# Performance work log

Hardware: AMD Instinct MI355X
Metric: run time of the kernel (lower is better)

The kernel has to match this reference:

```python
import jax, jax.numpy as jnp
import numpy as np

B, T, D, H, K = 2, 2048, 1024, 16, 4
DH = D // H  # 64 head dim
EPS_L2 = 1e-6
EPS_RMS = 1e-6


def setup_inputs() -> dict:
    key = jax.random.key(0)
    ks = jax.random.split(key, 10)
    s = 0.02
    return {
        'x': jax.random.normal(ks[0], (B, T, D), jnp.float32),
        'Wq': jax.random.normal(ks[1], (D, D), jnp.float32) * s,
        'Wk': jax.random.normal(ks[2], (D, D), jnp.float32) * s,
        'Wv': jax.random.normal(ks[3], (D, D), jnp.float32) * s,
        'Wb': jax.random.normal(ks[4], (D, H), jnp.float32) * s,
        'conv_q': jax.random.normal(ks[5], (D, K), jnp.float32) * 0.5,
        'conv_k': jax.random.normal(ks[6], (D, K), jnp.float32) * 0.5,
        'conv_v': jax.random.normal(ks[7], (D, K), jnp.float32) * 0.5,
        'rms_g': jnp.ones((DH,), jnp.float32),
        'Wo': jax.random.normal(ks[8], (D, D), jnp.float32) * s,
    }


def _silu(u):
    return u * jax.nn.sigmoid(u)


def _short_conv(x, w):
    # causal depthwise conv1d, x: [B,T,C], w: [C,K]; y[t] = sum_i w[:,i]*x[t-(K-1)+i]
    k = w.shape[1]
    xp = jnp.pad(x, ((0, 0), (k - 1, 0), (0, 0)))
    y = xp[:, 0:T, :] * w[:, 0]
    for i in range(1, k):
        y = y + xp[:, i:i + T, :] * w[:, i]
    return y


def _l2norm(u):
    return u * jax.lax.rsqrt(jnp.sum(u * u, axis=-1, keepdims=True) + EPS_L2)


def reference(x, Wq, Wk, Wv, Wb, conv_q, conv_k, conv_v, rms_g, Wo):
    # projections + causal short conv (silu fused, as in fla ShortConvolution)
    q = _silu(_short_conv(x @ Wq, conv_q)).reshape(B, T, H, DH)
    k = _silu(_short_conv(x @ Wk, conv_k)).reshape(B, T, H, DH)
    v = _silu(_short_conv(x @ Wv, conv_v)).reshape(B, T, H, DH)
    q = _l2norm(q)
    k = _l2norm(k)
    beta = jax.nn.sigmoid(x @ Wb)  # [B,T,H]

    # time-major for scan
    qs = q.transpose(1, 0, 2, 3)  # [T,B,H,DH]
    ks_ = k.transpose(1, 0, 2, 3)
    vs = v.transpose(1, 0, 2, 3)
    bs = beta.transpose(1, 0, 2)  # [T,B,H]

    def step(S, inp):
        # S: [B,H,dk,dv]; delta rule: S <- S + beta * k (v - k^T S)^T
        q_t, k_t, v_t, b_t = inp
        kS = jnp.einsum('bhk,bhkv->bhv', k_t, S)
        S = S + jnp.einsum('bhk,bhv->bhkv', k_t, b_t[..., None] * (v_t - kS))
        o_t = jnp.einsum('bhk,bhkv->bhv', q_t, S)
        return S, o_t

    S0 = jnp.zeros((B, H, DH, DH), x.dtype)
    _, o = jax.lax.scan(step, S0, (qs, ks_, vs, bs))  # o: [T,B,H,DH]
    o = o.transpose(1, 0, 2, 3)  # [B,T,H,DH]

    # per-head RMSNorm then output projection
    o = o * jax.lax.rsqrt(jnp.mean(o * o, axis=-1, keepdims=True) + EPS_RMS) * rms_g
    return o.reshape(B, T, D) @ Wo
```

## Files before the change

### kernel.cpp

```cpp
#include <hip/hip_runtime.h>
#include <hip/hip_bf16.h>
#include <math.h>

#define B_ 2
#define T_ 2048
#define D_ 1024
#define H_ 16
#define DH_ 64
#define M_ (B_*T_)
#define NC_ 32
#define CS_ 64
#define NCH_ (B_*H_*NC_)
#define QKVN_ 3072

typedef __attribute__((ext_vector_type(4))) float floatx4;
typedef __attribute__((ext_vector_type(8))) short short8;

__device__ __forceinline__ ushort f2bf(float f) {
  union { float f; unsigned u; } c; c.f = f;
  unsigned r = (c.u + 0x7FFFu + ((c.u >> 16) & 1u)) >> 16;
  return (ushort)r;
}
__device__ __forceinline__ float siluf(float u) {
  return u / (1.f + __expf(-u));
}
__device__ __forceinline__ float f4get(const float4& v, int j) {
  return j == 0 ? v.x : j == 1 ? v.y : j == 2 ? v.z : v.w;
}
__device__ __forceinline__ float rdlane(float v, int l) {
  return __int_as_float(__builtin_amdgcn_readlane(__float_as_int(v), l));
}
__device__ __forceinline__ int ksw(int r, int c) { return ((c ^ (r >> 4)) << 2); }

__global__ void cast_kernel(const float* __restrict__ in, ushort* __restrict__ out, int n4) {
  int i = blockIdx.x * blockDim.x + threadIdx.x;
  if (i >= n4) return;
  float4 v = ((const float4*)in)[i];
  ushort4 o;
  o.x = f2bf(v.x); o.y = f2bf(v.y); o.z = f2bf(v.z); o.w = f2bf(v.w);
  ((ushort4*)out)[i] = o;
}

__global__ void transpose_cast_kernel(const float* __restrict__ W, ushort* __restrict__ Wt,
                                      int K, int N) {
  __shared__ float tile[32][33];
  int tx = threadIdx.x, ty = threadIdx.y;
  int n0 = blockIdx.x * 32, k0 = blockIdx.y * 32;
  #pragma unroll
  for (int i = 0; i < 32; i += 8)
    tile[ty + i][tx] = W[(size_t)(k0 + ty + i) * N + n0 + tx];
  __syncthreads();
  #pragma unroll
  for (int i = 0; i < 32; i += 8)
    Wt[(size_t)(n0 + ty + i) * K + k0 + tx] = f2bf(tile[tx][ty + i]);
}

__global__ void transpose_wb_kernel(const float* __restrict__ Wb, float* __restrict__ WbT) {
  int bk = blockIdx.x;
  int tid = threadIdx.x;
  int kl = tid >> 4, h = tid & 15;
  int k = bk * 16 + kl;
  WbT[(size_t)h * D_ + k] = Wb[(size_t)k * H_ + h];
}

__global__ __launch_bounds__(256) void gemm128_kernel(
    const ushort* __restrict__ A, const ushort* __restrict__ Bt,
    float* __restrict__ C, int M, int N, int K) {
  __shared__ ushort lA[128 * 32];
  __shared__ ushort lB[128 * 32];
  int tid = threadIdx.x;
  int wave = tid >> 6, lane = tid & 63;
  int wm = wave >> 1, wn = wave & 1;
  int m16 = lane & 15, q4 = lane >> 4;
  int bm = blockIdx.x, bn = blockIdx.y;
  floatx4 acc[4][4] = {};
  int srow = tid >> 2;
  int sk8 = tid & 3;
  const ushort* Ag = A + (size_t)(bm * 128 + srow) * K + sk8 * 8;
  const ushort* Bg = Bt + (size_t)(bn * 128 + srow) * K + sk8 * 8;
  ushort* lAp = lA + tid * 8;
  ushort* lBp = lB + tid * 8;
  for (int k0 = 0; k0 < K; k0 += 32) {
    __builtin_amdgcn_global_load_lds(
        (const __attribute__((address_space(1))) void*)(Ag + k0),
        (__attribute__((address_space(3))) void*)lAp, 16, 0, 0);
    __builtin_amdgcn_global_load_lds(
        (const __attribute__((address_space(1))) void*)(Ag + (size_t)64 * K + k0),
        (__attribute__((address_space(3))) void*)(lAp + 2048), 16, 0, 0);
    __builtin_amdgcn_global_load_lds(
        (const __attribute__((address_space(1))) void*)(Bg + k0),
        (__attribute__((address_space(3))) void*)lBp, 16, 0, 0);
    __builtin_amdgcn_global_load_lds(
        (const __attribute__((address_space(1))) void*)(Bg + (size_t)64 * K + k0),
        (__attribute__((address_space(3))) void*)(lBp + 2048), 16, 0, 0);
    __syncthreads();
    short8 af[4], bf[4];
    #pragma unroll
    for (int i = 0; i < 4; i++) {
      af[i] = *(short8*)&lA[(wm * 64 + i * 16 + m16) * 32 + q4 * 8];
      bf[i] = *(short8*)&lB[(wn * 64 + i * 16 + m16) * 32 + q4 * 8];
    }
    #pragma unroll
    for (int mi = 0; mi < 4; mi++)
      #pragma unroll
      for (int nj = 0; nj < 4; nj++)
        acc[mi][nj] = __builtin_amdgcn_mfma_f32_16x16x32_bf16(af[mi], bf[nj], acc[mi][nj], 0, 0, 0);
    __syncthreads();
  }
  float* Cb = C + (size_t)(bm * 128) * N + bn * 128;
  #pragma unroll
  for (int mi = 0; mi < 4; mi++) {
    #pragma unroll
    for (int nj = 0; nj < 4; nj++) {
      #pragma unroll
      for (int i = 0; i < 4; i++) {
        int row = wm * 64 + mi * 16 + q4 * 4 + i;
        int col = wn * 64 + nj * 16 + m16;
        Cb[(size_t)row * N + col] = acc[mi][nj][i];
      }
    }
  }
}

__global__ __launch_bounds__(256) void beta_kernel(const float* __restrict__ x,
                                                   const float* __restrict__ WbT,
                                                   float* __restrict__ beta) {
  __shared__ __align__(16) float xs[D_];
  int row = blockIdx.x;
  int tid = threadIdx.x;
  ((float4*)xs)[tid] = ((const float4*)(x + (size_t)row * D_))[tid];
  __syncthreads();
  int h = tid >> 4;
  int seg = tid & 15;
  const float4* wrow = (const float4*)(WbT + (size_t)h * D_) + seg * 16;
  const float4* xsrow = (const float4*)xs + seg * 16;
  float s = 0.f;
  #pragma unroll
  for (int j = 0; j < 16; j++) {
    int jj = (j + seg) & 15;
    float4 xv = xsrow[jj];
    float4 wv = wrow[jj];
    s += xv.x * wv.x + xv.y * wv.y + xv.z * wv.z + xv.w * wv.w;
  }
  #pragma unroll
  for (int off = 8; off; off >>= 1) s += __shfl_down(s, off, 16);
  if (seg == 0) beta[(size_t)row * H_ + h] = 1.f / (1.f + __expf(-s));
}

__global__ __launch_bounds__(256) void conv_kernel(
    const float* __restrict__ qkv,
    const float* __restrict__ cq, const float* __restrict__ ck, const float* __restrict__ cv,
    float* __restrict__ qo, float* __restrict__ ko, float* __restrict__ vo) {
  int row = blockIdx.x;
  int t = row & (T_ - 1);
  int tid = threadIdx.x;
  int c0 = tid * 4;
  float4 zf = {0.f, 0.f, 0.f, 0.f};
  float4 xq[4], xk[4], xv[4];
  #pragma unroll
  for (int i = 0; i < 4; i++) {
    int tt = t - 3 + i;
    if (tt >= 0) {
      const float* rp = qkv + (size_t)(row - 3 + i) * QKVN_;
      xq[i] = *(const float4*)(rp + c0);
      xk[i] = *(const float4*)(rp + 1024 + c0);
      xv[i] = *(const float4*)(rp + 2048 + c0);
    } else { xq[i] = zf; xk[i] = zf; xv[i] = zf; }
  }
  float yq[4], yk[4], yv[4];
  float pq = 0.f, pk = 0.f;
  #pragma unroll
  for (int j = 0; j < 4; j++) {
    float4 wq = ((const float4*)cq)[c0 + j];
    float4 wk = ((const float4*)ck)[c0 + j];
    float4 wv = ((const float4*)cv)[c0 + j];
    float sq = 0.f, sk = 0.f, sv = 0.f;
    #pragma unroll
    for (int i = 0; i < 4; i++) {
      sq += f4get(wq, i) * f4get(xq[i], j);
      sk += f4get(wk, i) * f4get(xk[i], j);
      sv += f4get(wv, i) * f4get(xv[i], j);
    }
    yq[j] = siluf(sq); yk[j] = siluf(sk); yv[j] = siluf(sv);
    pq += yq[j] * yq[j]; pk += yk[j] * yk[j];
  }
  #pragma unroll
  for (int off = 1; off < 16; off <<= 1) {
    pq += __shfl_xor(pq, off, 16);
    pk += __shfl_xor(pk, off, 16);
  }
  float rq = rsqrtf(pq + 1e-6f), rk = rsqrtf(pk + 1e-6f);
  float4 oq = {yq[0]*rq, yq[1]*rq, yq[2]*rq, yq[3]*rq};
  float4 okk = {yk[0]*rk, yk[1]*rk, yk[2]*rk, yk[3]*rk};
  float4 ov = {yv[0], yv[1], yv[2], yv[3]};
  *(float4*)(qo + (size_t)row * D_ + c0) = oq;
  *(float4*)(ko + (size_t)row * D_ + c0) = okk;
  *(float4*)(vo + (size_t)row * D_ + c0) = ov;
}

__global__ __launch_bounds__(256) void prep1_kernel(
    const float* __restrict__ kn, const float* __restrict__ vn,
    const float* __restrict__ beta,
    float* __restrict__ Wkbuf, float* __restrict__ U0buf) {
  __shared__ __align__(16) float Ash[64 * 68];
  __shared__ float bsh[64];
  __shared__ __align__(16) float uni[5312];
  float (*Ksh)[68] = (float (*)[68])uni;
  float (*Tsh)[16][20] = (float (*)[16][20])uni;
  float (*Msh)[16][20] = (float (*)[16][20])(uni + 1280);
  float (*Xsh)[132] = (float (*)[132])(uni + 3200);

  int ch = blockIdx.x;
  int b = ch >> 9, h = (ch >> 5) & 15, c = ch & 31;
  int tid = threadIdx.x;
  int t = tid >> 2, seg = tid & 3;
  int wave = tid >> 6, lane = tid & 63;
  int r = lane >> 2, q = lane & 3;
  const float* krow = kn + ((size_t)(b * T_ + c * 64 + t)) * D_ + h * 64;
  #pragma unroll
  for (int g = 0; g < 4; g++)
    *(float4*)&Ksh[t][ksw(t, seg * 4 + g)] = *(const float4*)&krow[seg * 16 + 4 * g];
  if (tid < 64) bsh[tid] = beta[((size_t)(b * T_ + c * 64 + tid)) * H_ + h];
  __syncthreads();
  {
    int s0 = seg * 16;
    float acc[16];
    #pragma unroll
    for (int rr = 0; rr < 16; rr++) acc[rr] = 0.f;
    for (int d4 = 0; d4 < 16; d4++) {
      float4 kt = *(float4*)&Ksh[t][ksw(t, d4)];
      #pragma unroll
      for (int rr = 0; rr < 16; rr++) {
        float4 ks = *(float4*)&Ksh[s0 + rr][((d4 ^ seg) << 2)];
        acc[rr] += kt.x * ks.x + kt.y * ks.y + kt.z * ks.z + kt.w * ks.w;
      }
    }
    float bt = bsh[t];
    #pragma unroll
    for (int g = 0; g < 4; g++) {
      float4 a4;
      a4.x = (t > s0 + 4*g + 0) ? bt * acc[4*g+0] : 0.f;
      a4.y = (t > s0 + 4*g + 1) ? bt * acc[4*g+1] : 0.f;
      a4.z = (t > s0 + 4*g + 2) ? bt * acc[4*g+2] : 0.f;
      a4.w = (t > s0 + 4*g + 3) ? bt * acc[4*g+3] : 0.f;
      *(float4*)&Ash[t * 68 + s0 + 4 * g] = a4;
    }
  }
  float xk[16], xv[16];
  {
    float bt = bsh[t];
    const float* vrow = vn + ((size_t)(b * T_ + c * 64 + t)) * D_ + h * 64;
    #pragma unroll
    for (int g = 0; g < 4; g++) {
      float4 kv = *(float4*)&Ksh[t][ksw(t, seg * 4 + g)];
      float4 vv = *(const float4*)&vrow[seg * 16 + 4 * g];
      xk[4*g+0] = bt * kv.x; xk[4*g+1] = bt * kv.y; xk[4*g+2] = bt * kv.z; xk[4*g+3] = bt * kv.w;
      xv[4*g+0] = bt * vv.x; xv[4*g+1] = bt * vv.y; xv[4*g+2] = bt * vv.z; xv[4*g+3] = bt * vv.w;
    }
  }
  __syncthreads();
  {
    float a[16];
    #pragma unroll
    for (int i = 0; i < 16; i++) a[i] = Ash[(wave * 16 + r) * 68 + wave * 16 + i];
    float4 w4 = {0.f, 0.f, 0.f, 0.f};
    if ((r >> 2) == q) ((float*)&w4)[r & 3] = 1.f;
    #pragma unroll
    for (int i = 0; i < 15; i++) {
      int src = i * 4 + q;
      float4 wi;
      wi.x = __shfl(w4.x, src, 64);
      wi.y = __shfl(w4.y, src, 64);
      wi.z = __shfl(w4.z, src, 64);
      wi.w = __shfl(w4.w, src, 64);
      if (r > i) {
        w4.x -= a[i] * wi.x; w4.y -= a[i] * wi.y;
        w4.z -= a[i] * wi.z; w4.w -= a[i] * wi.w;
      }
    }
    *(float4*)&Tsh[wave][r][q * 4] = w4;
  }
  __syncthreads();
  for (int k = 0; k < wave; k++) {
    float4 m4 = {0.f, 0.f, 0.f, 0.f};
    #pragma unroll
    for (int i = 0; i < 16; i++) {
      float aik = Ash[(wave * 16 + r) * 68 + k * 16 + i];
      float4 tk = *(float4*)&Tsh[k][i][q * 4];
      m4.x += aik * tk.x; m4.y += aik * tk.y;
      m4.z += aik * tk.z; m4.w += aik * tk.w;
    }
    int mi = wave * (wave - 1) / 2 + k;
    *(float4*)&Msh[mi][r][q * 4] = m4;
  }
  float* wkout = &Wkbuf[(size_t)ch * 4096 + t * 64];
  float* u0out = &U0buf[(size_t)ch * 4096 + t * 64];
  for (int k = 0; k < 4; k++) {
    if (wave == k) {
      #pragma unroll
      for (int g = 0; g < 4; g++) {
        float4 k4 = {xk[4*g+0], xk[4*g+1], xk[4*g+2], xk[4*g+3]};
        float4 v4 = {xv[4*g+0], xv[4*g+1], xv[4*g+2], xv[4*g+3]};
        *(float4*)&Xsh[r][seg * 16 + 4 * g] = k4;
        *(float4*)&Xsh[r][64 + seg * 16 + 4 * g] = v4;
      }
    }
    __syncthreads();
    if (wave == k) {
      float nk[16], nv[16];
      #pragma unroll
      for (int i2 = 0; i2 < 16; i2++) { nk[i2] = 0.f; nv[i2] = 0.f; }
      #pragma unroll
      for (int i = 0; i < 16; i++) {
        float tc = Tsh[k][r][i];
        #pragma unroll
        for (int g = 0; g < 4; g++) {
          float4 yk = *(float4*)&Xsh[i][seg * 16 + 4 * g];
          float4 yv = *(float4*)&Xsh[i][64 + seg * 16 + 4 * g];
          nk[4*g+0] += tc * yk.x; nk[4*g+1] += tc * yk.y;
          nk[4*g+2] += tc * yk.z; nk[4*g+3] += tc * yk.w;
          nv[4*g+0] += tc * yv.x; nv[4*g+1] += tc * yv.y;
          nv[4*g+2] += tc * yv.z; nv[4*g+3] += tc * yv.w;
        }
      }
      #pragma unroll
      for (int g = 0; g < 4; g++) {
        float4 k4 = {nk[4*g+0], nk[4*g+1], nk[4*g+2], nk[4*g+3]};
        float4 v4 = {nv[4*g+0], nv[4*g+1], nv[4*g+2], nv[4*g+3]};
        *(float4*)&wkout[seg * 16 + 4 * g] = k4;
        *(float4*)&u0out[seg * 16 + 4 * g] = v4;
      }
    } else if (wave > k) {
      int mi = wave * (wave - 1) / 2 + k;
      #pragma unroll
      for (int i = 0; i < 16; i++) {
        float mc = Msh[mi][r][i];
        #pragma unroll
        for (int g = 0; g < 4; g++) {
          float4 yk = *(float4*)&Xsh[i][seg * 16 + 4 * g];
          float4 yv = *(float4*)&Xsh[i][64 + seg * 16 + 4 * g];
          xk[4*g+0] -= mc * yk.x; xk[4*g+1] -= mc * yk.y;
          xk[4*g+2] -= mc * yk.z; xk[4*g+3] -= mc * yk.w;
          xv[4*g+0] -= mc * yv.x; xv[4*g+1] -= mc * yv.y;
          xv[4*g+2] -= mc * yv.z; xv[4*g+3] -= mc * yv.w;
        }
      }
    }
    __syncthreads();
  }
}

__global__ __launch_bounds__(256) void prep2a_kernel(
    const float* __restrict__ qn, const float* __restrict__ kn,
    float* __restrict__ Lbuf) {
  __shared__ float Qsh[64][68];
  __shared__ float Ksh[64][68];
  int ch = blockIdx.x;
  int b = ch >> 9, h = (ch >> 5) & 15, c = ch & 31;
  int tid = threadIdx.x;
  int t = tid >> 2, seg = tid & 3;
  const float* qrow = qn + ((size_t)(b * T_ + c * 64 + t)) * D_ + h * 64;
  const float* krow = kn + ((size_t)(b * T_ + c * 64 + t)) * D_ + h * 64;
  #pragma unroll
  for (int g = 0; g < 4; g++) {
    *(float4*)&Qsh[t][seg * 16 + 4 * g] = *(const float4*)&qrow[seg * 16 + 4 * g];
    *(float4*)&Ksh[t][ksw(t, seg * 4 + g)] = *(const float4*)&krow[seg * 16 + 4 * g];
  }
  __syncthreads();
  int s0 = seg * 16;
  float acc[16];
  #pragma unroll
  for (int r = 0; r < 16; r++) acc[r] = 0.f;
  for (int d4 = 0; d4 < 16; d4++) {
    float4 qt = *(float4*)&Qsh[t][d4 * 4];
    #pragma unroll
    for (int r = 0; r < 16; r++) {
      float4 ks = *(float4*)&Ksh[s0 + r][((d4 ^ seg) << 2)];
      acc[r] += qt.x * ks.x + qt.y * ks.y + qt.z * ks.z + qt.w * ks.w;
    }
  }
  #pragma unroll
  for (int g = 0; g < 4; g++) {
    float4 ov;
    ov.x = (s0 + 4*g + 0 <= t) ? acc[4*g+0] : 0.f;
    ov.y = (s0 + 4*g + 1 <= t) ? acc[4*g+1] : 0.f;
    ov.z = (s0 + 4*g + 2 <= t) ? acc[4*g+2] : 0.f;
    ov.w = (s0 + 4*g + 3 <= t) ? acc[4*g+3] : 0.f;
    *(float4*)&Lbuf[(size_t)ch * 4096 + t * 64 + s0 + 4 * g] = ov;
  }
}

__global__ __launch_bounds__(256) void prep2b_kernel(
    const float* __restrict__ Lbuf, const float* __restrict__ Wkbuf,
    const float* __restrict__ U0buf, float* qn,
    float* __restrict__ O0buf) {
  __shared__ float Lsh[64][68];
  __shared__ float Wksh[64][68];
  __shared__ float U0sh[64][68];
  int ch = blockIdx.x;
  int b = ch >> 9, h = (ch >> 5) & 15, c = ch & 31;
  int tid = threadIdx.x;
  int t = tid >> 2, seg = tid & 3;
  #pragma unroll
  for (int g = 0; g < 4; g++) {
    int o = t * 64 + seg * 16 + 4 * g;
    *(float4*)&Lsh[t][seg * 16 + 4 * g]  = *(const float4*)&Lbuf[(size_t)ch * 4096 + o];
    *(float4*)&Wksh[t][seg * 16 + 4 * g] = *(const float4*)&Wkbuf[(size_t)ch * 4096 + o];
    *(float4*)&U0sh[t][seg * 16 + 4 * g] = *(const float4*)&U0buf[(size_t)ch * 4096 + o];
  }
  __syncthreads();
  int j0 = seg * 16;
  float o0[16], lw[16];
  #pragma unroll
  for (int r = 0; r < 16; r++) { o0[r] = 0.f; lw[r] = 0.f; }
  for (int s = 0; s <= t; s++) {
    float l = Lsh[t][s];
    #pragma unroll
    for (int g = 0; g < 4; g++) {
      float4 u = *(float4*)&U0sh[s][j0 + 4 * g];
      float4 w = *(float4*)&Wksh[s][j0 + 4 * g];
      o0[4*g+0] += l * u.x; o0[4*g+1] += l * u.y; o0[4*g+2] += l * u.z; o0[4*g+3] += l * u.w;
      lw[4*g+0] += l * w.x; lw[4*g+1] += l * w.y; lw[4*g+2] += l * w.z; lw[4*g+3] += l * w.w;
    }
  }
  float* qrow = qn + ((size_t)(b * T_ + c * 64 + t)) * D_ + h * 64;
  #pragma unroll
  for (int g = 0; g < 4; g++) {
    float4 qv = *(const float4*)&qrow[j0 + 4 * g];
    qv.x -= lw[4*g+0]; qv.y -= lw[4*g+1]; qv.z -= lw[4*g+2]; qv.w -= lw[4*g+3];
    *(float4*)&qrow[j0 + 4 * g] = qv;
    float4 ov = {o0[4*g+0], o0[4*g+1], o0[4*g+2], o0[4*g+3]};
    *(float4*)&O0buf[(size_t)ch * 4096 + t * 64 + j0 + 4 * g] = ov;
  }
}

__global__ __launch_bounds__(256) void prep2c_kernel(
    float* kn, const float* __restrict__ Wkbuf,
    const float* __restrict__ U0buf, float* __restrict__ Pbuf) {
  __shared__ float Ksh[64][68];
  __shared__ float Wksh[64][68];
  __shared__ float U0sh[64][68];
  int ch = blockIdx.x;
  int b = ch >> 9, h = (ch >> 5) & 15, c = ch & 31;
  int tid = threadIdx.x;
  int t = tid >> 2, seg = tid & 3;
  const float* krow = kn + ((size_t)(b * T_ + c * 64 + t)) * D_ + h * 64;
  #pragma unroll
  for (int g = 0; g < 4; g++) {
    int o = t * 64 + seg * 16 + 4 * g;
    *(float4*)&Ksh[t][seg * 16 + 4 * g]  = *(const float4*)&krow[seg * 16 + 4 * g];
    *(float4*)&Wksh[t][seg * 16 + 4 * g] = *(const float4*)&Wkbuf[(size_t)ch * 4096 + o];
    *(float4*)&U0sh[t][seg * 16 + 4 * g] = *(const float4*)&U0buf[(size_t)ch * 4096 + o];
  }
  __syncthreads();
  int d0 = seg * 16;
  float accP[16], accZ[16];
  #pragma unroll
  for (int r = 0; r < 16; r++) { accP[r] = 0.f; accZ[r] = 0.f; }
  for (int s = 0; s < 64; s++) {
    float kt = Ksh[s][t];
    float u  = U0sh[s][t];
    #pragma unroll
    for (int g = 0; g < 4; g++) {
      float4 w4 = *(float4*)&Wksh[s][d0 + 4 * g];
      float4 k4 = *(float4*)&Ksh[s][d0 + 4 * g];
      accP[4*g+0] += kt * w4.x; accP[4*g+1] += kt * w4.y; accP[4*g+2] += kt * w4.z; accP[4*g+3] += kt * w4.w;
      accZ[4*g+0] += u * k4.x;  accZ[4*g+1] += u * k4.y;  accZ[4*g+2] += u * k4.z;  accZ[4*g+3] += u * k4.w;
    }
  }
  float* zrow = kn + ((size_t)(b * T_ + c * 64 + t)) * D_ + h * 64;
  #pragma unroll
  for (int g = 0; g < 4; g++) {
    float4 pv;
    pv.x = ((d0 + 4*g + 0) == t ? 1.f : 0.f) - accP[4*g+0];
    pv.y = ((d0 + 4*g + 1) == t ? 1.f : 0.f) - accP[4*g+1];
    pv.z = ((d0 + 4*g + 2) == t ? 1.f : 0.f) - accP[4*g+2];
    pv.w = ((d0 + 4*g + 3) == t ? 1.f : 0.f) - accP[4*g+3];
    *(float4*)&Pbuf[(size_t)ch * 4096 + (size_t)(seg * 4 + g) * 256 + (size_t)t * 4] = pv;
    float4 zv = {accZ[4*g+0], accZ[4*g+1], accZ[4*g+2], accZ[4*g+3]};
    *(float4*)&zrow[d0 + 4 * g] = zv;
  }
}

__global__ __launch_bounds__(256) void state_kernel(
    const float* __restrict__ kn , const float* __restrict__ Pbuf ,
    float* __restrict__ Sbuf) {
  __shared__ __align__(16) float Pl[2][4096];
  int bid = blockIdx.x;
  int bh = bid & 31, js = bid >> 5;
  int h = bh & 15, b = bh >> 4;
  int tid = threadIdx.x;
  int wv = tid >> 6, lane = tid & 63;
  int j0 = js * 4 + wv;
  float s0 = 0.f;
  const size_t bhNC = (size_t)bh * NC_;
  const float* Pg0 = Pbuf + bhNC * 4096;
  #pragma unroll
  for (int g = 0; g < 4; g++)
    __builtin_amdgcn_global_load_lds(
        (const __attribute__((address_space(1))) void*)(Pg0 + (g * 256 + tid) * 4),
        (__attribute__((address_space(3))) void*)&Pl[0][(g * 256 + tid) * 4], 16, 0, 0);
  float zn = kn[((size_t)(b * T_ + j0)) * D_ + h * 64 + lane];
  int cur = 0;
  #pragma unroll 1
  for (int c = 0; c < NC_; c++) {
    __syncthreads();
    float z = zn;
    size_t ch = bhNC + c;
    if (c + 1 < NC_) {
      const float* Pg = Pbuf + (ch + 1) * 4096;
      #pragma unroll
      for (int g = 0; g < 4; g++)
        __builtin_amdgcn_global_load_lds(
            (const __attribute__((address_space(1))) void*)(Pg + (g * 256 + tid) * 4),
            (__attribute__((address_space(3))) void*)&Pl[cur ^ 1][(g * 256 + tid) * 4], 16, 0, 0);
      zn = kn[((size_t)(b * T_ + (c + 1) * 64 + j0)) * D_ + h * 64 + lane];
    }
    Sbuf[ch * 4096 + (size_t)j0 * 64 + lane] = s0;
    float acc = z;
    #pragma unroll
    for (int f = 0; f < 16; f++) {
      floatx4 pv = *(floatx4*)&Pl[cur][f * 256 + lane * 4];
      acc += pv.x * rdlane(s0, f * 4 + 0);
      acc += pv.y * rdlane(s0, f * 4 + 1);
      acc += pv.z * rdlane(s0, f * 4 + 2);
      acc += pv.w * rdlane(s0, f * 4 + 3);
    }
    s0 = acc;
    cur ^= 1;
  }
}

__global__ __launch_bounds__(256) void ophase_kernel(
    const float* __restrict__ qn , const float* __restrict__ Sbuf,
    const float* __restrict__ O0buf, const float* __restrict__ rms_g,
    ushort* __restrict__ ob) {
  __shared__ float Ssht[64][68];
  __shared__ float QshT[64][65];
  __shared__ float part[64][4];
  int ch = blockIdx.x;
  int b = ch >> 9, h = (ch >> 5) & 15, c = ch & 31;
  int tid = threadIdx.x;
  int t = tid & 63, jg = tid >> 6;
  #pragma unroll
  for (int g = 0; g < 4; g++) {
    int idx = tid + g * 256;
    *(float4*)&Ssht[idx >> 4][(idx & 15) * 4] =
        *(const float4*)&Sbuf[(size_t)ch * 4096 + (size_t)idx * 4];
  }
  #pragma unroll
  for (int g = 0; g < 4; g++) {
    int idx = tid + g * 256;
    int row = idx >> 4, c4 = idx & 15;
    float4 qv = *(const float4*)&qn[((size_t)(b * T_ + c * 64 + row)) * D_ + h * 64 + c4 * 4];
    QshT[c4 * 4 + 0][row] = qv.x;
    QshT[c4 * 4 + 1][row] = qv.y;
    QshT[c4 * 4 + 2][row] = qv.z;
    QshT[c4 * 4 + 3][row] = qv.w;
  }
  float o[16];
  #pragma unroll
  for (int g = 0; g < 4; g++) {
    float4 o4 = *(const float4*)&O0buf[(size_t)ch * 4096 + t * 64 + jg * 16 + g * 4];
    o[4*g+0] = o4.x; o[4*g+1] = o4.y; o[4*g+2] = o4.z; o[4*g+3] = o4.w;
  }
  __syncthreads();
  for (int d4 = 0; d4 < 16; d4++) {
    float q0 = QshT[d4 * 4 + 0][t];
    float q1 = QshT[d4 * 4 + 1][t];
    float q2 = QshT[d4 * 4 + 2][t];
    float q3 = QshT[d4 * 4 + 3][t];
    #pragma unroll
    for (int r = 0; r < 16; r++) {
      float4 s4 = *(float4*)&Ssht[jg * 16 + r][d4 * 4];
      o[r] += q0 * s4.x + q1 * s4.y + q2 * s4.z + q3 * s4.w;
    }
  }
  float ss = 0.f;
  #pragma unroll
  for (int r = 0; r < 16; r++) ss += o[r] * o[r];
  part[t][jg] = ss;
  __syncthreads();
  float tot = part[t][0] + part[t][1] + part[t][2] + part[t][3];
  float sc = rsqrtf(tot * (1.f / 64.f) + 1e-6f);
  ushort* orow = &ob[((size_t)(b * T_ + c * 64 + t)) * D_ + h * 64];
  #pragma unroll
  for (int g = 0; g < 4; g++) {
    float4 g4 = *(const float4*)&rms_g[jg * 16 + g * 4];
    ushort4 r4;
    r4.x = f2bf(o[4*g+0] * sc * g4.x); r4.y = f2bf(o[4*g+1] * sc * g4.y);
    r4.z = f2bf(o[4*g+2] * sc * g4.z); r4.w = f2bf(o[4*g+3] * sc * g4.w);
    *(ushort4*)&orow[jg * 16 + g * 4] = r4;
  }
}

extern "C" void kernel_launch(void* const* d_in, const int* in_sizes, int n_in,
                              void* d_out, int out_size, void* d_ws, size_t ws_size,
                              hipStream_t stream) {
  const float* x  = (const float*)d_in[0];
  const float* Wq = (const float*)d_in[1];
  const float* Wk = (const float*)d_in[2];
  const float* Wv = (const float*)d_in[3];
  const float* Wb = (const float*)d_in[4];
  const float* cq = (const float*)d_in[5];
  const float* ck = (const float*)d_in[6];
  const float* cv = (const float*)d_in[7];
  const float* rg = (const float*)d_in[8];
  const float* Wo = (const float*)d_in[9];
  float* out = (float*)d_out;
  char* ws = (char*)d_ws;
  const size_t MiB = 1ull << 20;
  ushort* xb   = (ushort*)(ws + 0);
  ushort* Wqt  = (ushort*)(ws + 8 * MiB);
  ushort* Wkt  = (ushort*)(ws + 10 * MiB);
  ushort* Wvt  = (ushort*)(ws + 12 * MiB);
  ushort* Wot  = (ushort*)(ws + 14 * MiB);
  float* qkv   = (float*)(ws + 16 * MiB);
  float* qn    = (float*)(ws + 64 * MiB);
  float* kn    = (float*)(ws + 80 * MiB);
  float* vn    = (float*)(ws + 96 * MiB);
  float* beta  = (float*)(ws + 112 * MiB);
  float* WbT   = (float*)(ws + 112 * MiB + 256 * 1024);
  float* Wkbuf = (float*)(ws + 16 * MiB);
  float* U0buf = (float*)(ws + 32 * MiB);
  float* Lbuf  = (float*)(ws + 48 * MiB);
  float* O0buf = (float*)(ws + 96 * MiB);
  float* Sbuf  = (float*)(ws + 16 * MiB);
  ushort* ob   = (ushort*)(ws + 0);

  hipLaunchKernelGGL(cast_kernel, dim3(M_ * D_ / 4 / 256), dim3(256), 0, stream,
                     x, xb, M_ * D_ / 4);
  dim3 tb(32, 8);
  hipLaunchKernelGGL(transpose_cast_kernel, dim3(32, 32), tb, 0, stream, Wq, Wqt, D_, D_);
  hipLaunchKernelGGL(transpose_cast_kernel, dim3(32, 32), tb, 0, stream, Wk, Wkt, D_, D_);
  hipLaunchKernelGGL(transpose_cast_kernel, dim3(32, 32), tb, 0, stream, Wv, Wvt, D_, D_);
  hipLaunchKernelGGL(transpose_cast_kernel, dim3(32, 32), tb, 0, stream, Wo, Wot, D_, D_);
  hipLaunchKernelGGL(transpose_wb_kernel, dim3(64), dim3(256), 0, stream, Wb, WbT);

  hipLaunchKernelGGL(gemm128_kernel, dim3(M_ / 128, QKVN_ / 128), dim3(256), 0, stream,
                     xb, Wqt, qkv, M_, QKVN_, D_);

  hipLaunchKernelGGL(beta_kernel, dim3(M_), dim3(256), 0, stream, x, WbT, beta);
  hipLaunchKernelGGL(conv_kernel, dim3(M_), dim3(256), 0, stream,
                     qkv, cq, ck, cv, qn, kn, vn);

  hipLaunchKernelGGL(prep1_kernel, dim3(NCH_), dim3(256), 0, stream,
                     kn, vn, beta, Wkbuf, U0buf);
  hipLaunchKernelGGL(prep2a_kernel, dim3(NCH_), dim3(256), 0, stream, qn, kn, Lbuf);
  hipLaunchKernelGGL(prep2b_kernel, dim3(NCH_), dim3(256), 0, stream,
                     Lbuf, Wkbuf, U0buf, qn, O0buf);
  hipLaunchKernelGGL(prep2c_kernel, dim3(NCH_), dim3(256), 0, stream,
                     kn, Wkbuf, U0buf, Lbuf);
  hipLaunchKernelGGL(state_kernel, dim3(512), dim3(256), 0, stream,
                     kn, Lbuf, Sbuf);
  hipLaunchKernelGGL(ophase_kernel, dim3(NCH_), dim3(256), 0, stream,
                     qn, Sbuf, O0buf, rg, ob);
  hipLaunchKernelGGL(gemm128_kernel, dim3(M_ / 128, D_ / 128), dim3(256), 0, stream,
                     ob, Wot, out, M_, D_, D_);
}
```

Before: 406.5 us.

## Fuse intra-chunk QK^T mask kernel into the prep2b solve kernel

Merges prep2a and prep2b into one kernel. The causally masked Q·K^T chunk matrix L is kept in shared memory instead of being written to a global buffer and read back. The Wk and U0 tiles reuse the Q and K shared buffers once L has been computed. This removes one kernel launch and a round trip of about 16 MiB through global memory, in exchange for an extra barrier and higher shared-memory use in the fused kernel.

```diff
diff --git a/kernel.cpp b/kernel.cpp
--- a/kernel.cpp
+++ b/kernel.cpp
@@ -350,11 +350,15 @@
   }
 }
 
-__global__ __launch_bounds__(256) void prep2a_kernel(
-    const float* __restrict__ qn, const float* __restrict__ kn,
-    float* __restrict__ Lbuf) {
+__global__ __launch_bounds__(256) void prep2ab_kernel(
+    float* qn, const float* __restrict__ kn,
+    const float* __restrict__ Wkbuf, const float* __restrict__ U0buf,
+    float* __restrict__ O0buf) {
   __shared__ float Qsh[64][68];
   __shared__ float Ksh[64][68];
+  __shared__ float Lsh[64][68];
+  float (*Wksh)[68] = Qsh;
+  float (*U0sh)[68] = Ksh;
   int ch = blockIdx.x;
   int b = ch >> 9, h = (ch >> 5) & 15, c = ch & 31;
   int tid = threadIdx.x;
@@ -367,44 +371,33 @@
     *(float4*)&Ksh[t][ksw(t, seg * 4 + g)] = *(const float4*)&krow[seg * 16 + 4 * g];
   }
   __syncthreads();
-  int s0 = seg * 16;
-  float acc[16];
-  #pragma unroll
-  for (int r = 0; r < 16; r++) acc[r] = 0.f;
-  for (int d4 = 0; d4 < 16; d4++) {
-    float4 qt = *(float4*)&Qsh[t][d4 * 4];
-    #pragma unroll
-    for (int r = 0; r < 16; r++) {
-      float4 ks = *(float4*)&Ksh[s0 + r][((d4 ^ seg) << 2)];
-      acc[r] += qt.x * ks.x + qt.y * ks.y + qt.z * ks.z + qt.w * ks.w;
-    }
-  }
-  #pragma unroll
-  for (int g = 0; g < 4; g++) {
-    float4 ov;
-    ov.x = (s0 + 4*g + 0 <= t) ? acc[4*g+0] : 0.f;
-    ov.y = (s0 + 4*g + 1 <= t) ? acc[4*g+1] : 0.f;
-    ov.z = (s0 + 4*g + 2 <= t) ? acc[4*g+2] : 0.f;
-    ov.w = (s0 + 4*g + 3 <= t) ? acc[4*g+3] : 0.f;
-    *(float4*)&Lbuf[(size_t)ch * 4096 + t * 64 + s0 + 4 * g] = ov;
-  }
-}
-
-__global__ __launch_bounds__(256) void prep2b_kernel(
-    const float* __restrict__ Lbuf, const float* __restrict__ Wkbuf,
-    const float* __restrict__ U0buf, float* qn,
-    float* __restrict__ O0buf) {
-  __shared__ float Lsh[64][68];
-  __shared__ float Wksh[64][68];
-  __shared__ float U0sh[64][68];
-  int ch = blockIdx.x;
-  int b = ch >> 9, h = (ch >> 5) & 15, c = ch & 31;
-  int tid = threadIdx.x;
-  int t = tid >> 2, seg = tid & 3;
+  {
+    int s0 = seg * 16;
+    float acc[16];
+    #pragma unroll
+    for (int r = 0; r < 16; r++) acc[r] = 0.f;
+    for (int d4 = 0; d4 < 16; d4++) {
+      float4 qt = *(float4*)&Qsh[t][d4 * 4];
+      #pragma unroll
+      for (int r = 0; r < 16; r++) {
+        float4 ks = *(float4*)&Ksh[s0 + r][((d4 ^ seg) << 2)];
+        acc[r] += qt.x * ks.x + qt.y * ks.y + qt.z * ks.z + qt.w * ks.w;
+      }
+    }
+    #pragma unroll
+    for (int g = 0; g < 4; g++) {
+      float4 ov;
+      ov.x = (s0 + 4*g + 0 <= t) ? acc[4*g+0] : 0.f;
+      ov.y = (s0 + 4*g + 1 <= t) ? acc[4*g+1] : 0.f;
+      ov.z = (s0 + 4*g + 2 <= t) ? acc[4*g+2] : 0.f;
+      ov.w = (s0 + 4*g + 3 <= t) ? acc[4*g+3] : 0.f;
+      *(float4*)&Lsh[t][s0 + 4 * g] = ov;
+    }
+  }
+  __syncthreads();
   #pragma unroll
   for (int g = 0; g < 4; g++) {
     int o = t * 64 + seg * 16 + 4 * g;
-    *(float4*)&Lsh[t][seg * 16 + 4 * g]  = *(const float4*)&Lbuf[(size_t)ch * 4096 + o];
     *(float4*)&Wksh[t][seg * 16 + 4 * g] = *(const float4*)&Wkbuf[(size_t)ch * 4096 + o];
     *(float4*)&U0sh[t][seg * 16 + 4 * g] = *(const float4*)&U0buf[(size_t)ch * 4096 + o];
   }
@@ -423,12 +416,12 @@
       lw[4*g+0] += l * w.x; lw[4*g+1] += l * w.y; lw[4*g+2] += l * w.z; lw[4*g+3] += l * w.w;
     }
   }
-  float* qrow = qn + ((size_t)(b * T_ + c * 64 + t)) * D_ + h * 64;
-  #pragma unroll
-  for (int g = 0; g < 4; g++) {
-    float4 qv = *(const float4*)&qrow[j0 + 4 * g];
+  float* qwrow = qn + ((size_t)(b * T_ + c * 64 + t)) * D_ + h * 64;
+  #pragma unroll
+  for (int g = 0; g < 4; g++) {
+    float4 qv = *(const float4*)&qwrow[j0 + 4 * g];
     qv.x -= lw[4*g+0]; qv.y -= lw[4*g+1]; qv.z -= lw[4*g+2]; qv.w -= lw[4*g+3];
-    *(float4*)&qrow[j0 + 4 * g] = qv;
+    *(float4*)&qwrow[j0 + 4 * g] = qv;
     float4 ov = {o0[4*g+0], o0[4*g+1], o0[4*g+2], o0[4*g+3]};
     *(float4*)&O0buf[(size_t)ch * 4096 + t * 64 + j0 + 4 * g] = ov;
   }
@@ -623,7 +616,7 @@
   float* WbT   = (float*)(ws + 112 * MiB + 256 * 1024);
   float* Wkbuf = (float*)(ws + 16 * MiB);
   float* U0buf = (float*)(ws + 32 * MiB);
-  float* Lbuf  = (float*)(ws + 48 * MiB);
+  float* Pbuf  = (float*)(ws + 48 * MiB);
   float* O0buf = (float*)(ws + 96 * MiB);
   float* Sbuf  = (float*)(ws + 16 * MiB);
   ushort* ob   = (ushort*)(ws + 0);
@@ -646,13 +639,12 @@
 
   hipLaunchKernelGGL(prep1_kernel, dim3(NCH_), dim3(256), 0, stream,
                      kn, vn, beta, Wkbuf, U0buf);
-  hipLaunchKernelGGL(prep2a_kernel, dim3(NCH_), dim3(256), 0, stream, qn, kn, Lbuf);
-  hipLaunchKernelGGL(prep2b_kernel, dim3(NCH_), dim3(256), 0, stream,
-                     Lbuf, Wkbuf, U0buf, qn, O0buf);
+  hipLaunchKernelGGL(prep2ab_kernel, dim3(NCH_), dim3(256), 0, stream,
+                     qn, kn, Wkbuf, U0buf, O0buf);
   hipLaunchKernelGGL(prep2c_kernel, dim3(NCH_), dim3(256), 0, stream,
-                     kn, Wkbuf, U0buf, Lbuf);
+                     kn, Wkbuf, U0buf, Pbuf);
   hipLaunchKernelGGL(state_kernel, dim3(512), dim3(256), 0, stream,
-                     kn, Lbuf, Sbuf);
+                     kn, Pbuf, Sbuf);
   hipLaunchKernelGGL(ophase_kernel, dim3(NCH_), dim3(256), 0, stream,
                      qn, Sbuf, O0buf, rg, ob);
   hipLaunchKernelGGL(gemm128_kernel, dim3(M_ / 128, D_ / 128), dim3(256), 0, stream,
```

Result: faster. 397.6 us (-2.2%).
